# Optimization experiments

Hardware: AMD Instinct MI355X
Metric: run time of the kernel (lower is better)

The kernel has to match this reference:

```python
import jax, jax.numpy as jnp
import numpy as np

B, S, D = 2, 4096, 512
H = 8
HD = D // H


def setup_inputs() -> dict:
    key = jax.random.key(0)
    k1, k2, k3, k4, k5 = jax.random.split(key, 5)
    sd = 1.0 / np.sqrt(D)
    return {
        "x": jax.random.normal(k1, (B, S, D), dtype=jnp.float32),
        "Wqkv": jax.random.normal(k2, (3 * D, D), dtype=jnp.float32) * sd,
        "bqkv": jax.random.normal(k3, (3 * D,), dtype=jnp.float32) * 0.02,
        "Wo": jax.random.normal(k4, (D, D), dtype=jnp.float32) * sd,
        "bo": jax.random.normal(k5, (D,), dtype=jnp.float32) * 0.02,
    }


def reference(x, Wqkv, bqkv, Wo, bo):
    b, s, d = x.shape
    h, hd = H, d // H
    # QKV projection (torch Linear: x @ W^T + b)
    qkv = x @ Wqkv.T + bqkv                      # [b, s, 3d]
    q, k, v = jnp.split(qkv, 3, axis=-1)         # each [b, s, d]
    # [b, s, h, hd] -> [b, h, s, hd]
    q = q.reshape(b, s, h, hd).transpose(0, 2, 1, 3)
    k = k.reshape(b, s, h, hd).transpose(0, 2, 1, 3)
    v = v.reshape(b, s, h, hd).transpose(0, 2, 1, 3)
    # causal additive mask: triu(ones, diag=1) * -1e10
    mask = jnp.triu(jnp.ones((s, s), dtype=x.dtype), k=1) * jnp.asarray(-1e10, x.dtype)
    wts = jnp.einsum("bhqd,bhkd->bhqk", q, k) / np.sqrt(hd).astype(np.float32)
    wts = wts + mask[None, None, :, :]
    wts = jax.nn.softmax(wts, axis=-1)
    y = jnp.einsum("bhqk,bhkd->bhqd", wts, v)    # [b, h, s, hd]
    y = y.transpose(0, 2, 1, 3).reshape(b, s, d) # [b, s, d]
    out = y @ Wo.T + bo
    return out
```

## Files before the change

kernel.cpp:

```cpp
#include <hip/hip_runtime.h>


typedef __bf16 bf16x8 __attribute__((ext_vector_type(8)));
typedef float f32x4 __attribute__((ext_vector_type(4)));
typedef unsigned short u16;

#define MFMA(a, b, c) __builtin_amdgcn_mfma_f32_16x16x32_bf16(a, b, c, 0, 0, 0)
#define QSCALE 0.18033688011112042f

__device__ __forceinline__ float exp2_fast(float x) {
    return __builtin_amdgcn_exp2f(x);
}
__device__ __forceinline__ u16 f2bf(float f) {
    union { __bf16 h; u16 u; } v; v.h = (__bf16)f; return v.u;
}
__device__ __forceinline__ ushort4 f4_to_bf4(float4 v) {
    ushort4 r;
    r.x = f2bf(v.x); r.y = f2bf(v.y); r.z = f2bf(v.z); r.w = f2bf(v.w);
    return r;
}
__device__ __forceinline__ void load_lds16(const u16* g, u16* l) {
    __builtin_amdgcn_global_load_lds(
        (const __attribute__((address_space(1))) void*)g,
        (__attribute__((address_space(3))) void*)l, 16, 0, 0);
}

__global__ __launch_bounds__(256) void cvt_all(
    const float* __restrict__ x, const float* __restrict__ wq,
    const float* __restrict__ wo,
    u16* __restrict__ xb, u16* __restrict__ wqb, u16* __restrict__ wob)
{
    int i = blockIdx.x * 256 + threadIdx.x;
    if (i < 1048576) {
        ((ushort4*)xb)[i] = f4_to_bf4(((const float4*)x)[i]);
    } else if (i < 1048576 + 196608) {
        int j = i - 1048576;
        ((ushort4*)wqb)[j] = f4_to_bf4(((const float4*)wq)[j]);
    } else {
        int j = i - 1048576 - 196608;
        ((ushort4*)wob)[j] = f4_to_bf4(((const float4*)wo)[j]);
    }
}

__global__ __launch_bounds__(256) void gemm_qkv_bf(
    const u16* __restrict__ X, const u16* __restrict__ W,
    const float* __restrict__ bias,
    u16* __restrict__ QY, u16* __restrict__ Ko, u16* __restrict__ Vto)
{
    __shared__ u16 As[2 * 128 * 32];
    __shared__ u16 Bs[2 * 128 * 32];
    const int K = 512;
    const int tid = threadIdx.x, wave = tid >> 6, lane = tid & 63;
    const int l15 = lane & 15, quad = lane >> 4;
    const int bm = blockIdx.x * 128, bn = blockIdx.y * 128;
    const int wr = wave >> 1, wc = wave & 1;
    const int arow = lane >> 2;
    const int acol = (lane & 3) * 8;

    f32x4 acc[4][4] = {};
#pragma unroll
    for (int ii = 0; ii < 2; ii++) {
        const int inst = wave * 2 + ii;
        const int row = inst * 16 + arow;
        load_lds16(&X[(bm + row) * K + acol], &As[inst * 512]);
        load_lds16(&W[(bn + row) * K + acol], &Bs[inst * 512]);
    }
    int cur = 0;
    for (int k0 = 0; k0 < K; k0 += 32) {
        __builtin_amdgcn_s_barrier();
        if (k0 + 32 < K) {
            const int nb = (cur ^ 1) * 4096;
#pragma unroll
            for (int ii = 0; ii < 2; ii++) {
                const int inst = wave * 2 + ii;
                const int row = inst * 16 + arow;
                load_lds16(&X[(bm + row) * K + k0 + 32 + acol], &As[nb + inst * 512]);
                load_lds16(&W[(bn + row) * K + k0 + 32 + acol], &Bs[nb + inst * 512]);
            }
            asm volatile("s_waitcnt vmcnt(4)" ::: "memory");
        } else {
            asm volatile("s_waitcnt vmcnt(0)" ::: "memory");
        }
        __builtin_amdgcn_s_barrier();
        const int cb = cur * 4096;
        bf16x8 a[4], b[4];
#pragma unroll
        for (int i = 0; i < 4; i++)
            a[i] = *(const bf16x8*)&As[cb + (wr * 64 + i * 16 + l15) * 32 + quad * 8];
#pragma unroll
        for (int j = 0; j < 4; j++)
            b[j] = *(const bf16x8*)&Bs[cb + (wc * 64 + j * 16 + l15) * 32 + quad * 8];
#pragma unroll
        for (int i = 0; i < 4; i++)
#pragma unroll
            for (int j = 0; j < 4; j++)
                acc[i][j] = MFMA(b[i], a[j], acc[i][j]);
        cur ^= 1;
    }

    const int nbase = bn + wc * 64;
    const int which = nbase >> 9;
#pragma unroll
    for (int i = 0; i < 4; i++) {
        const int d0 = nbase + i * 16 + quad * 4;
        const float4 bv = *(const float4*)&bias[d0];
        const int d0m = d0 & 511;
        const int h = d0m >> 6, hd0 = d0m & 63;
#pragma unroll
        for (int j = 0; j < 4; j++) {
            const int s_g = bm + wr * 64 + j * 16 + l15;
            const int b_ = s_g >> 12, s0 = s_g & 4095;
            const int bhh = b_ * 8 + h;
            if (which == 2) {
#pragma unroll
                for (int r = 0; r < 4; r++) {
                    const float bvr = (r == 0) ? bv.x : (r == 1) ? bv.y : (r == 2) ? bv.z : bv.w;
                    Vto[((size_t)(bhh * 64 + hd0 + r)) * 4096 + s0] = f2bf(acc[i][j][r] + bvr);
                }
            } else if (which == 1) {
                ushort4 pk;
                pk.x = f2bf(acc[i][j][0] + bv.x);
                pk.y = f2bf(acc[i][j][1] + bv.y);
                pk.z = f2bf(acc[i][j][2] + bv.z);
                pk.w = f2bf(acc[i][j][3] + bv.w);
                *(ushort4*)&Ko[(bhh * 4096 + s0) * 64 + hd0] = pk;
            } else {
                ushort4 pk;
                pk.x = f2bf((acc[i][j][0] + bv.x) * QSCALE);
                pk.y = f2bf((acc[i][j][1] + bv.y) * QSCALE);
                pk.z = f2bf((acc[i][j][2] + bv.z) * QSCALE);
                pk.w = f2bf((acc[i][j][3] + bv.w) * QSCALE);
                *(ushort4*)&QY[((b_ * 4096 + s0) * 8 + h) * 64 + hd0] = pk;
            }
        }
    }
}

#define LS 72

__global__ __launch_bounds__(128, 4) void attn_k(
    const u16* __restrict__ QY, const u16* __restrict__ Kk, const u16* __restrict__ Vt,
    u16* __restrict__ PO, float* __restrict__ ML)
{
    __shared__ u16 Ks[2 * 64 * 64];
    __shared__ u16 Vs[64 * 64];
    __shared__ u16 Ps[2 * 16 * LS];

    const int tid = threadIdx.x, wave = tid >> 6, lane = tid & 63;
    const int l15 = lane & 15, quad = lane >> 4;
    const int bh = blockIdx.x;
    const int b_ = bh >> 3, h = bh & 7;
    const int y = (int)blockIdx.y;
    const int qt = 63 - (y >> 1);
    const int seg = y & 1;
    const int total = qt + 1;
    const int half = (total + 1) >> 1;
    const int kt0 = seg ? half : 0;
    const int kt1 = seg ? total : half;
    const int base_r = qt * 64 + wave * 32;

    const u16* qpa = &QY[((b_ * 4096 + base_r + l15) * 8 + h) * 64];
    const u16* qpb = qpa + 16 * 8 * 64;
    bf16x8 qa0 = *(const bf16x8*)&qpa[quad * 8];
    bf16x8 qa1 = *(const bf16x8*)&qpa[32 + quad * 8];
    bf16x8 qb0 = *(const bf16x8*)&qpb[quad * 8];
    bf16x8 qb1 = *(const bf16x8*)&qpb[32 + quad * 8];

    f32x4 oa[4] = {}, ob[4] = {};
    f32x4 lacc_a = {}, lacc_b = {};

    const int sr = lane >> 3;
    const int swz = 8 * ((lane & 7) ^ sr);
    const u16* KgA = &Kk[(size_t)bh * 4096 * 64 + (wave * 32 + sr) * 64 + swz];
    const u16* VgA = &Vt[(size_t)bh * 64 * 4096 + (wave * 32 + sr) * 4096 + swz];
    u16* KsW = &Ks[wave * 2048];
    u16* VsW = &Vs[wave * 2048];

    const int c0 = 8 * (quad ^ (l15 & 7));

    bf16x8 ones;
#pragma unroll
    for (int i = 0; i < 8; i++) ones[i] = (__bf16)1.0f;

    u16* P = &Ps[wave * 16 * LS];

#pragma unroll
    for (int i = 0; i < 4; i++)
        load_lds16(KgA + kt0 * 4096 + i * 512, KsW + i * 512);

    int cur = 0;
    for (int kt = kt0; kt < kt1; kt++) {
        const int k0 = kt * 64;
        __builtin_amdgcn_s_barrier();
#pragma unroll
        for (int i = 0; i < 4; i++)
            load_lds16(VgA + k0 + i * 32768, VsW + i * 512);
        const bool havnext = (kt + 1 < kt1);
        if (havnext) {
            u16* kb = &Ks[(cur ^ 1) * 4096 + wave * 2048];
#pragma unroll
            for (int i = 0; i < 4; i++)
                load_lds16(KgA + (kt + 1) * 4096 + i * 512, kb + i * 512);
            asm volatile("s_waitcnt vmcnt(8)" ::: "memory");
        } else {
            asm volatile("s_waitcnt vmcnt(4)" ::: "memory");
        }
        __builtin_amdgcn_s_barrier();

        const u16* Kcur = &Ks[cur * 4096];
        const bool nmA = (k0 + 63 > base_r);
        const bool nmB = (k0 + 63 > base_r + 16);
        f32x4 sa[4], sb[4];
#pragma unroll
        for (int j = 0; j < 4; j++) {
            f32x4 ia = {}, ib = {};
            if (nmA) {
#pragma unroll
                for (int r = 0; r < 4; r++) {
                    const int key = k0 + j * 16 + quad * 4 + r;
                    ia[r] = (key > base_r + l15) ? -1e30f : 0.0f;
                }
            }
            if (nmB) {
#pragma unroll
                for (int r = 0; r < 4; r++) {
                    const int key = k0 + j * 16 + quad * 4 + r;
                    ib[r] = (key > base_r + 16 + l15) ? -1e30f : 0.0f;
                }
            }
            const int kb = (j * 16 + l15) * 64;
            bf16x8 kf0 = *(const bf16x8*)&Kcur[kb + c0];
            bf16x8 kf1 = *(const bf16x8*)&Kcur[kb + (c0 ^ 32)];
            ia = MFMA(kf0, qa0, ia);
            sa[j] = MFMA(kf1, qa1, ia);
            ib = MFMA(kf0, qb0, ib);
            sb[j] = MFMA(kf1, qb1, ib);
        }

        {
            float spa[4][4];
#pragma unroll
            for (int j = 0; j < 4; j++)
#pragma unroll
                for (int r = 0; r < 4; r++)
                    spa[j][r] = exp2_fast(sa[j][r]);
#pragma unroll
            for (int j = 0; j < 4; j++) {
                ushort4 w;
                w.x = f2bf(spa[j][0]); w.y = f2bf(spa[j][1]);
                w.z = f2bf(spa[j][2]); w.w = f2bf(spa[j][3]);
                *(ushort4*)&P[l15 * LS + j * 16 + quad * 4] = w;
            }
        }

        float spb[4][4];
#pragma unroll
        for (int j = 0; j < 4; j++)
#pragma unroll
            for (int r = 0; r < 4; r++)
                spb[j][r] = exp2_fast(sb[j][r]);

        bf16x8 pfa0 = *(const bf16x8*)&P[l15 * LS + quad * 8];
        bf16x8 pfa1 = *(const bf16x8*)&P[l15 * LS + 32 + quad * 8];
#pragma unroll
        for (int j = 0; j < 4; j++) {
            ushort4 w;
            w.x = f2bf(spb[j][0]); w.y = f2bf(spb[j][1]);
            w.z = f2bf(spb[j][2]); w.w = f2bf(spb[j][3]);
            *(ushort4*)&P[l15 * LS + j * 16 + quad * 4] = w;
        }
        bf16x8 pfb0 = *(const bf16x8*)&P[l15 * LS + quad * 8];
        bf16x8 pfb1 = *(const bf16x8*)&P[l15 * LS + 32 + quad * 8];

        lacc_a = MFMA(ones, pfa0, lacc_a);
        lacc_a = MFMA(ones, pfa1, lacc_a);
        lacc_b = MFMA(ones, pfb0, lacc_b);
        lacc_b = MFMA(ones, pfb1, lacc_b);

        if (havnext) {
            asm volatile("s_waitcnt vmcnt(4)" ::: "memory");
        } else {
            asm volatile("s_waitcnt vmcnt(0)" ::: "memory");
        }
        __builtin_amdgcn_s_barrier();

#pragma unroll
        for (int n = 0; n < 4; n++) {
            const int vb = (n * 16 + l15) * 64;
            bf16x8 vf0 = *(const bf16x8*)&Vs[vb + c0];
            bf16x8 vf1 = *(const bf16x8*)&Vs[vb + (c0 ^ 32)];
            oa[n] = MFMA(vf0, pfa0, oa[n]);
            oa[n] = MFMA(vf1, pfa1, oa[n]);
            ob[n] = MFMA(vf0, pfb0, ob[n]);
            ob[n] = MFMA(vf1, pfb1, ob[n]);
        }
        cur ^= 1;
    }

    const float lfa = lacc_a[0];
    const float lfb = lacc_b[0];
    const float iva = (lfa > 0.0f) ? 1.0f / lfa : 0.0f;
    const float ivb = (lfb > 0.0f) ? 1.0f / lfb : 0.0f;
    u16* ppa = &PO[(size_t)seg * 4194304 +
                   (size_t)((b_ * 4096 + base_r + l15) * 8 + h) * 64];
    u16* ppb = ppa + 16 * 8 * 64;
#pragma unroll
    for (int n = 0; n < 4; n++) {
        ushort4 wa;
        wa.x = f2bf(oa[n][0] * iva);
        wa.y = f2bf(oa[n][1] * iva);
        wa.z = f2bf(oa[n][2] * iva);
        wa.w = f2bf(oa[n][3] * iva);
        *(ushort4*)&ppa[n * 16 + quad * 4] = wa;
        ushort4 wb;
        wb.x = f2bf(ob[n][0] * ivb);
        wb.y = f2bf(ob[n][1] * ivb);
        wb.z = f2bf(ob[n][2] * ivb);
        wb.w = f2bf(ob[n][3] * ivb);
        *(ushort4*)&ppb[n * 16 + quad * 4] = wb;
    }
    if (quad == 0) {
        float* mpa = &ML[((seg * 16 + bh) * 4096 + base_r + l15) * 2];
        mpa[0] = 0.0f;
        mpa[1] = lfa;
        float* mpb = mpa + 16 * 2;
        mpb[0] = 0.0f;
        mpb[1] = lfb;
    }
}

__global__ __launch_bounds__(256) void merge_k(
    const u16* __restrict__ PO, const float* __restrict__ ML, u16* __restrict__ Y)
{
    const int flat = blockIdx.x * 256 + threadIdx.x;
    const int rs = flat >> 6;
    const int rem = flat & 63;
    const int h = rem >> 3, c = rem & 7;
    const int b_ = rs >> 12, s = rs & 4095;
    const int bh = b_ * 8 + h;
    const float m0 = ML[(bh * 4096 + s) * 2];
    const float l0 = ML[(bh * 4096 + s) * 2 + 1];
    const float m1 = ML[((16 + bh) * 4096 + s) * 2];
    const float l1 = ML[((16 + bh) * 4096 + s) * 2 + 1];
    const float m = fmaxf(m0, m1);
    const float w0 = (l0 > 0.0f) ? exp2_fast(m0 - m) * l0 : 0.0f;
    const float w1 = (l1 > 0.0f) ? exp2_fast(m1 - m) * l1 : 0.0f;
    const float inv = 1.0f / (w0 + w1);
    const float a0 = w0 * inv, a1 = w1 * inv;

    const size_t base = (size_t)(rs * 8 + h) * 64 + c * 8;
    bf16x8 x0 = *(const bf16x8*)&PO[base];
    bf16x8 x1 = *(const bf16x8*)&PO[4194304 + base];
    ushort4 lo, hi;
    lo.x = f2bf(a0 * (float)x0[0] + a1 * (float)x1[0]);
    lo.y = f2bf(a0 * (float)x0[1] + a1 * (float)x1[1]);
    lo.z = f2bf(a0 * (float)x0[2] + a1 * (float)x1[2]);
    lo.w = f2bf(a0 * (float)x0[3] + a1 * (float)x1[3]);
    hi.x = f2bf(a0 * (float)x0[4] + a1 * (float)x1[4]);
    hi.y = f2bf(a0 * (float)x0[5] + a1 * (float)x1[5]);
    hi.z = f2bf(a0 * (float)x0[6] + a1 * (float)x1[6]);
    hi.w = f2bf(a0 * (float)x0[7] + a1 * (float)x1[7]);
    *(ushort4*)&Y[base] = lo;
    *(ushort4*)&Y[base + 4] = hi;
}

__global__ __launch_bounds__(256) void gemm_o_bf(
    const u16* __restrict__ X, const u16* __restrict__ W,
    const float* __restrict__ bias, float* __restrict__ Out)
{
    __shared__ u16 As[2 * 128 * 32];
    __shared__ u16 Bs[2 * 128 * 32];
    const int K = 512;
    const int tid = threadIdx.x, wave = tid >> 6, lane = tid & 63;
    const int l15 = lane & 15, quad = lane >> 4;
    const int bm = blockIdx.x * 128, bn = blockIdx.y * 128;
    const int wr = wave >> 1, wc = wave & 1;
    const int arow = lane >> 2;
    const int acol = (lane & 3) * 8;

    f32x4 acc[4][4] = {};
#pragma unroll
    for (int ii = 0; ii < 2; ii++) {
        const int inst = wave * 2 + ii;
        const int row = inst * 16 + arow;
        load_lds16(&X[(bm + row) * K + acol], &As[inst * 512]);
        load_lds16(&W[(bn + row) * K + acol], &Bs[inst * 512]);
    }
    int cur = 0;
    for (int k0 = 0; k0 < K; k0 += 32) {
        __builtin_amdgcn_s_barrier();
        if (k0 + 32 < K) {
            const int nb = (cur ^ 1) * 4096;
#pragma unroll
            for (int ii = 0; ii < 2; ii++) {
                const int inst = wave * 2 + ii;
                const int row = inst * 16 + arow;
                load_lds16(&X[(bm + row) * K + k0 + 32 + acol], &As[nb + inst * 512]);
                load_lds16(&W[(bn + row) * K + k0 + 32 + acol], &Bs[nb + inst * 512]);
            }
            asm volatile("s_waitcnt vmcnt(4)" ::: "memory");
        } else {
            asm volatile("s_waitcnt vmcnt(0)" ::: "memory");
        }
        __builtin_amdgcn_s_barrier();
        const int cb = cur * 4096;
        bf16x8 a[4], b[4];
#pragma unroll
        for (int i = 0; i < 4; i++)
            a[i] = *(const bf16x8*)&As[cb + (wr * 64 + i * 16 + l15) * 32 + quad * 8];
#pragma unroll
        for (int j = 0; j < 4; j++)
            b[j] = *(const bf16x8*)&Bs[cb + (wc * 64 + j * 16 + l15) * 32 + quad * 8];
#pragma unroll
        for (int i = 0; i < 4; i++)
#pragma unroll
            for (int j = 0; j < 4; j++)
                acc[i][j] = MFMA(b[i], a[j], acc[i][j]);
        cur ^= 1;
    }
#pragma unroll
    for (int i = 0; i < 4; i++) {
        const int n0 = bn + wc * 64 + i * 16 + quad * 4;
        const float4 bv = *(const float4*)&bias[n0];
#pragma unroll
        for (int j = 0; j < 4; j++) {
            const int m = bm + wr * 64 + j * 16 + l15;
            float4 ov;
            ov.x = acc[i][j][0] + bv.x;
            ov.y = acc[i][j][1] + bv.y;
            ov.z = acc[i][j][2] + bv.z;
            ov.w = acc[i][j][3] + bv.w;
            *(float4*)&Out[(size_t)m * 512 + n0] = ov;
        }
    }
}

extern "C" void kernel_launch(void* const* d_in, const int* in_sizes, int n_in,
                              void* d_out, int out_size, void* d_ws, size_t ws_size,
                              hipStream_t stream) {
    (void)in_sizes; (void)n_in; (void)out_size; (void)ws_size;
    const float* x    = (const float*)d_in[0];
    const float* Wqkv = (const float*)d_in[1];
    const float* bqkv = (const float*)d_in[2];
    const float* Wo   = (const float*)d_in[3];
    const float* bo   = (const float*)d_in[4];
    float* out = (float*)d_out;

    u16* qy_ws = (u16*)d_ws;
    u16* k_ws  = qy_ws + 4194304;
    u16* vt_ws = k_ws + 4194304;
    float* ml  = (float*)(vt_ws + 4194304);
    u16* wqkvb = (u16*)(ml + 262144);
    u16* wob   = wqkvb + 786432;
    u16* xb    = (u16*)d_out;
    u16* po    = (u16*)d_out;

    cvt_all<<<5120, 256, 0, stream>>>(x, Wqkv, Wo, xb, wqkvb, wob);
    gemm_qkv_bf<<<dim3(64, 12), 256, 0, stream>>>(xb, wqkvb, bqkv, qy_ws, k_ws, vt_ws);
    attn_k<<<dim3(16, 128), 128, 0, stream>>>(qy_ws, k_ws, vt_ws, po, ml);
    merge_k<<<2048, 256, 0, stream>>>(po, ml, qy_ws);
    gemm_o_bf<<<dim3(64, 4), 256, 0, stream>>>(qy_ws, wob, bo, out);
}
```

Baseline: 182.1 us.

## Store K/V in MFMA-fragment layout and load directly from global in single-wave attention

The QKV GEMM epilogue now writes K and V in a per-64-key-tile layout that matches the MFMA operand fragments, so each lane reads its fragments with contiguous 16-byte global loads. The attention kernel drops the LDS staging, double buffering and barriers, runs one wave per block, and gives each block two 32-row query tiles paired from opposite ends of the causal triangle to balance work. This removes LDS traffic and block synchronisation, but loses K/V reuse across waves and leaves global latency unhidden except by occupancy.

```diff
diff --git a/kernel.cpp b/kernel.cpp
--- a/kernel.cpp
+++ b/kernel.cpp
@@ -45,7 +45,7 @@
 __global__ __launch_bounds__(256) void gemm_qkv_bf(
     const u16* __restrict__ X, const u16* __restrict__ W,
     const float* __restrict__ bias,
-    u16* __restrict__ QY, u16* __restrict__ Ko, u16* __restrict__ Vto)
+    u16* __restrict__ QY, u16* __restrict__ Kf, u16* __restrict__ Vf)
 {
     __shared__ u16 As[2 * 128 * 32];
     __shared__ u16 Bs[2 * 128 * 32];
@@ -111,19 +111,30 @@
             const int s_g = bm + wr * 64 + j * 16 + l15;
             const int b_ = s_g >> 12, s0 = s_g & 4095;
             const int bhh = b_ * 8 + h;
+            const int kt = s0 >> 6;
             if (which == 2) {
+                const int kk = s0 & 63;
+                const int halfv = kk >> 5, qv = (kk >> 3) & 3, e = kk & 7;
+                const int n = hd0 >> 4;
+                const int lv0 = hd0 & 15;
+                const size_t tb = ((size_t)(bhh * 64 + kt)) * 4096 +
+                                  n * 1024 + halfv * 512 + qv * 128 + e;
 #pragma unroll
                 for (int r = 0; r < 4; r++) {
                     const float bvr = (r == 0) ? bv.x : (r == 1) ? bv.y : (r == 2) ? bv.z : bv.w;
-                    Vto[((size_t)(bhh * 64 + hd0 + r)) * 4096 + s0] = f2bf(acc[i][j][r] + bvr);
+                    Vf[tb + (lv0 + r) * 8] = f2bf(acc[i][j][r] + bvr);
                 }
             } else if (which == 1) {
+                const int jj = (s0 >> 4) & 3, lr = s0 & 15;
+                const int half = hd0 >> 5, q4 = (hd0 >> 3) & 3, e0 = hd0 & 7;
                 ushort4 pk;
                 pk.x = f2bf(acc[i][j][0] + bv.x);
                 pk.y = f2bf(acc[i][j][1] + bv.y);
                 pk.z = f2bf(acc[i][j][2] + bv.z);
                 pk.w = f2bf(acc[i][j][3] + bv.w);
-                *(ushort4*)&Ko[(bhh * 4096 + s0) * 64 + hd0] = pk;
+                const size_t off = ((size_t)(bhh * 64 + kt)) * 4096 +
+                                   jj * 1024 + half * 512 + q4 * 128 + lr * 8 + e0;
+                *(ushort4*)&Kf[off] = pk;
             } else {
                 ushort4 pk;
                 pk.x = f2bf((acc[i][j][0] + bv.x) * QSCALE);
@@ -138,194 +149,170 @@
 
 #define LS 72
 
-__global__ __launch_bounds__(128, 4) void attn_k(
-    const u16* __restrict__ QY, const u16* __restrict__ Kk, const u16* __restrict__ Vt,
+__global__ __launch_bounds__(64, 3) void attn_k(
+    const u16* __restrict__ QY, const u16* __restrict__ Kf, const u16* __restrict__ Vf,
     u16* __restrict__ PO, float* __restrict__ ML)
 {
-    __shared__ u16 Ks[2 * 64 * 64];
-    __shared__ u16 Vs[64 * 64];
-    __shared__ u16 Ps[2 * 16 * LS];
-
-    const int tid = threadIdx.x, wave = tid >> 6, lane = tid & 63;
+    __shared__ u16 Ps[16 * LS];
+
+    const int lane = threadIdx.x;
     const int l15 = lane & 15, quad = lane >> 4;
     const int bh = blockIdx.x;
     const int b_ = bh >> 3, h = bh & 7;
     const int y = (int)blockIdx.y;
-    const int qt = 63 - (y >> 1);
+    const int p = y >> 1;
     const int seg = y & 1;
-    const int total = qt + 1;
-    const int half = (total + 1) >> 1;
-    const int kt0 = seg ? half : 0;
-    const int kt1 = seg ? total : half;
-    const int base_r = qt * 64 + wave * 32;
-
-    const u16* qpa = &QY[((b_ * 4096 + base_r + l15) * 8 + h) * 64];
-    const u16* qpb = qpa + 16 * 8 * 64;
-    bf16x8 qa0 = *(const bf16x8*)&qpa[quad * 8];
-    bf16x8 qa1 = *(const bf16x8*)&qpa[32 + quad * 8];
-    bf16x8 qb0 = *(const bf16x8*)&qpb[quad * 8];
-    bf16x8 qb1 = *(const bf16x8*)&qpb[32 + quad * 8];
-
-    f32x4 oa[4] = {}, ob[4] = {};
-    f32x4 lacc_a = {}, lacc_b = {};
-
-    const int sr = lane >> 3;
-    const int swz = 8 * ((lane & 7) ^ sr);
-    const u16* KgA = &Kk[(size_t)bh * 4096 * 64 + (wave * 32 + sr) * 64 + swz];
-    const u16* VgA = &Vt[(size_t)bh * 64 * 4096 + (wave * 32 + sr) * 4096 + swz];
-    u16* KsW = &Ks[wave * 2048];
-    u16* VsW = &Vs[wave * 2048];
-
-    const int c0 = 8 * (quad ^ (l15 & 7));
 
     bf16x8 ones;
 #pragma unroll
     for (int i = 0; i < 8; i++) ones[i] = (__bf16)1.0f;
 
-    u16* P = &Ps[wave * 16 * LS];
-
-#pragma unroll
-    for (int i = 0; i < 4; i++)
-        load_lds16(KgA + kt0 * 4096 + i * 512, KsW + i * 512);
-
-    int cur = 0;
-    for (int kt = kt0; kt < kt1; kt++) {
-        const int k0 = kt * 64;
-        __builtin_amdgcn_s_barrier();
-#pragma unroll
-        for (int i = 0; i < 4; i++)
-            load_lds16(VgA + k0 + i * 32768, VsW + i * 512);
-        const bool havnext = (kt + 1 < kt1);
-        if (havnext) {
-            u16* kb = &Ks[(cur ^ 1) * 4096 + wave * 2048];
-#pragma unroll
-            for (int i = 0; i < 4; i++)
-                load_lds16(KgA + (kt + 1) * 4096 + i * 512, kb + i * 512);
-            asm volatile("s_waitcnt vmcnt(8)" ::: "memory");
-        } else {
-            asm volatile("s_waitcnt vmcnt(4)" ::: "memory");
-        }
-        __builtin_amdgcn_s_barrier();
-
-        const u16* Kcur = &Ks[cur * 4096];
-        const bool nmA = (k0 + 63 > base_r);
-        const bool nmB = (k0 + 63 > base_r + 16);
-        f32x4 sa[4], sb[4];
-#pragma unroll
-        for (int j = 0; j < 4; j++) {
-            f32x4 ia = {}, ib = {};
-            if (nmA) {
-#pragma unroll
-                for (int r = 0; r < 4; r++) {
-                    const int key = k0 + j * 16 + quad * 4 + r;
-                    ia[r] = (key > base_r + l15) ? -1e30f : 0.0f;
+    const u16* KfB = &Kf[((size_t)bh * 64) * 4096 + lane * 8];
+    const u16* VfB = &Vf[((size_t)bh * 64) * 4096 + lane * 8];
+    u16* P = Ps;
+
+    for (int phase = 0; phase < 2; phase++) {
+        const int qt32 = phase ? (127 - p) : p;
+        const int nt = (qt32 >> 1) + 1;
+        const int hlf = (nt + 1) >> 1;
+        const int t0 = seg ? hlf : 0;
+        const int t1 = seg ? nt : hlf;
+        const int base_r = qt32 * 32;
+
+        const u16* qpa = &QY[((b_ * 4096 + base_r + l15) * 8 + h) * 64];
+        const u16* qpb = qpa + 16 * 8 * 64;
+        bf16x8 qa0 = *(const bf16x8*)&qpa[quad * 8];
+        bf16x8 qa1 = *(const bf16x8*)&qpa[32 + quad * 8];
+        bf16x8 qb0 = *(const bf16x8*)&qpb[quad * 8];
+        bf16x8 qb1 = *(const bf16x8*)&qpb[32 + quad * 8];
+
+        f32x4 oa[4] = {}, ob[4] = {};
+        f32x4 lacc_a = {}, lacc_b = {};
+        const int rowA = base_r + l15;
+
+        for (int kt = t0; kt < t1; kt++) {
+            const int k0 = kt * 64;
+            const u16* kp = KfB + kt * 4096;
+
+            bf16x8 kf[4][2];
+#pragma unroll
+            for (int j = 0; j < 4; j++) {
+                kf[j][0] = *(const bf16x8*)&kp[j * 1024];
+                kf[j][1] = *(const bf16x8*)&kp[j * 1024 + 512];
+            }
+
+            const bool nmA = (k0 + 63 > base_r);
+            const bool nmB = (k0 + 63 > base_r + 16);
+            f32x4 sa[4], sb[4];
+#pragma unroll
+            for (int j = 0; j < 4; j++) {
+                f32x4 ia = {}, ib = {};
+                if (nmA) {
+#pragma unroll
+                    for (int r = 0; r < 4; r++) {
+                        const int key = k0 + j * 16 + quad * 4 + r;
+                        ia[r] = (key > rowA) ? -1e30f : 0.0f;
+                    }
                 }
-            }
-            if (nmB) {
-#pragma unroll
-                for (int r = 0; r < 4; r++) {
-                    const int key = k0 + j * 16 + quad * 4 + r;
-                    ib[r] = (key > base_r + 16 + l15) ? -1e30f : 0.0f;
+                if (nmB) {
+#pragma unroll
+                    for (int r = 0; r < 4; r++) {
+                        const int key = k0 + j * 16 + quad * 4 + r;
+                        ib[r] = (key > rowA + 16) ? -1e30f : 0.0f;
+                    }
                 }
-            }
-            const int kb = (j * 16 + l15) * 64;
-            bf16x8 kf0 = *(const bf16x8*)&Kcur[kb + c0];
-            bf16x8 kf1 = *(const bf16x8*)&Kcur[kb + (c0 ^ 32)];
-            ia = MFMA(kf0, qa0, ia);
-            sa[j] = MFMA(kf1, qa1, ia);
-            ib = MFMA(kf0, qb0, ib);
-            sb[j] = MFMA(kf1, qb1, ib);
-        }
-
-        {
-            float spa[4][4];
+                ia = MFMA(kf[j][0], qa0, ia);
+                sa[j] = MFMA(kf[j][1], qa1, ia);
+                ib = MFMA(kf[j][0], qb0, ib);
+                sb[j] = MFMA(kf[j][1], qb1, ib);
+            }
+
+            const u16* vp = VfB + kt * 4096;
+            bf16x8 vf[4][2];
+#pragma unroll
+            for (int n = 0; n < 4; n++) {
+                vf[n][0] = *(const bf16x8*)&vp[n * 1024];
+                vf[n][1] = *(const bf16x8*)&vp[n * 1024 + 512];
+            }
+
+            {
+                float spa[4][4];
+#pragma unroll
+                for (int j = 0; j < 4; j++)
+#pragma unroll
+                    for (int r = 0; r < 4; r++)
+                        spa[j][r] = exp2_fast(sa[j][r]);
+#pragma unroll
+                for (int j = 0; j < 4; j++) {
+                    ushort4 w;
+                    w.x = f2bf(spa[j][0]); w.y = f2bf(spa[j][1]);
+                    w.z = f2bf(spa[j][2]); w.w = f2bf(spa[j][3]);
+                    *(ushort4*)&P[l15 * LS + j * 16 + quad * 4] = w;
+                }
+            }
+            float spb[4][4];
 #pragma unroll
             for (int j = 0; j < 4; j++)
 #pragma unroll
                 for (int r = 0; r < 4; r++)
-                    spa[j][r] = exp2_fast(sa[j][r]);
+                    spb[j][r] = exp2_fast(sb[j][r]);
+
+            bf16x8 pfa0 = *(const bf16x8*)&P[l15 * LS + quad * 8];
+            bf16x8 pfa1 = *(const bf16x8*)&P[l15 * LS + 32 + quad * 8];
 #pragma unroll
             for (int j = 0; j < 4; j++) {
                 ushort4 w;
-                w.x = f2bf(spa[j][0]); w.y = f2bf(spa[j][1]);
-                w.z = f2bf(spa[j][2]); w.w = f2bf(spa[j][3]);
+                w.x = f2bf(spb[j][0]); w.y = f2bf(spb[j][1]);
+                w.z = f2bf(spb[j][2]); w.w = f2bf(spb[j][3]);
                 *(ushort4*)&P[l15 * LS + j * 16 + quad * 4] = w;
             }
-        }
-
-        float spb[4][4];
-#pragma unroll
-        for (int j = 0; j < 4; j++)
-#pragma unroll
-            for (int r = 0; r < 4; r++)
-                spb[j][r] = exp2_fast(sb[j][r]);
-
-        bf16x8 pfa0 = *(const bf16x8*)&P[l15 * LS + quad * 8];
-        bf16x8 pfa1 = *(const bf16x8*)&P[l15 * LS + 32 + quad * 8];
-#pragma unroll
-        for (int j = 0; j < 4; j++) {
-            ushort4 w;
-            w.x = f2bf(spb[j][0]); w.y = f2bf(spb[j][1]);
-            w.z = f2bf(spb[j][2]); w.w = f2bf(spb[j][3]);
-            *(ushort4*)&P[l15 * LS + j * 16 + quad * 4] = w;
-        }
-        bf16x8 pfb0 = *(const bf16x8*)&P[l15 * LS + quad * 8];
-        bf16x8 pfb1 = *(const bf16x8*)&P[l15 * LS + 32 + quad * 8];
-
-        lacc_a = MFMA(ones, pfa0, lacc_a);
-        lacc_a = MFMA(ones, pfa1, lacc_a);
-        lacc_b = MFMA(ones, pfb0, lacc_b);
-        lacc_b = MFMA(ones, pfb1, lacc_b);
-
-        if (havnext) {
-            asm volatile("s_waitcnt vmcnt(4)" ::: "memory");
-        } else {
-            asm volatile("s_waitcnt vmcnt(0)" ::: "memory");
-        }
-        __builtin_amdgcn_s_barrier();
-
+            bf16x8 pfb0 = *(const bf16x8*)&P[l15 * LS + quad * 8];
+            bf16x8 pfb1 = *(const bf16x8*)&P[l15 * LS + 32 + quad * 8];
+
+            lacc_a = MFMA(ones, pfa0, lacc_a);
+            lacc_a = MFMA(ones, pfa1, lacc_a);
+            lacc_b = MFMA(ones, pfb0, lacc_b);
+            lacc_b = MFMA(ones, pfb1, lacc_b);
+
+#pragma unroll
+            for (int n = 0; n < 4; n++) {
+                oa[n] = MFMA(vf[n][0], pfa0, oa[n]);
+                oa[n] = MFMA(vf[n][1], pfa1, oa[n]);
+                ob[n] = MFMA(vf[n][0], pfb0, ob[n]);
+                ob[n] = MFMA(vf[n][1], pfb1, ob[n]);
+            }
+        }
+
+        const float lfa = lacc_a[0];
+        const float lfb = lacc_b[0];
+        const float iva = (lfa > 0.0f) ? 1.0f / lfa : 0.0f;
+        const float ivb = (lfb > 0.0f) ? 1.0f / lfb : 0.0f;
+        u16* ppa = &PO[(size_t)seg * 4194304 +
+                       (size_t)((b_ * 4096 + base_r + l15) * 8 + h) * 64];
+        u16* ppb = ppa + 16 * 8 * 64;
 #pragma unroll
         for (int n = 0; n < 4; n++) {
-            const int vb = (n * 16 + l15) * 64;
-            bf16x8 vf0 = *(const bf16x8*)&Vs[vb + c0];
-            bf16x8 vf1 = *(const bf16x8*)&Vs[vb + (c0 ^ 32)];
-            oa[n] = MFMA(vf0, pfa0, oa[n]);
-            oa[n] = MFMA(vf1, pfa1, oa[n]);
-            ob[n] = MFMA(vf0, pfb0, ob[n]);
-            ob[n] = MFMA(vf1, pfb1, ob[n]);
-        }
-        cur ^= 1;
-    }
-
-    const float lfa = lacc_a[0];
-    const float lfb = lacc_b[0];
-    const float iva = (lfa > 0.0f) ? 1.0f / lfa : 0.0f;
-    const float ivb = (lfb > 0.0f) ? 1.0f / lfb : 0.0f;
-    u16* ppa = &PO[(size_t)seg * 4194304 +
-                   (size_t)((b_ * 4096 + base_r + l15) * 8 + h) * 64];
-    u16* ppb = ppa + 16 * 8 * 64;
-#pragma unroll
-    for (int n = 0; n < 4; n++) {
-        ushort4 wa;
-        wa.x = f2bf(oa[n][0] * iva);
-        wa.y = f2bf(oa[n][1] * iva);
-        wa.z = f2bf(oa[n][2] * iva);
-        wa.w = f2bf(oa[n][3] * iva);
-        *(ushort4*)&ppa[n * 16 + quad * 4] = wa;
-        ushort4 wb;
-        wb.x = f2bf(ob[n][0] * ivb);
-        wb.y = f2bf(ob[n][1] * ivb);
-        wb.z = f2bf(ob[n][2] * ivb);
-        wb.w = f2bf(ob[n][3] * ivb);
-        *(ushort4*)&ppb[n * 16 + quad * 4] = wb;
-    }
-    if (quad == 0) {
-        float* mpa = &ML[((seg * 16 + bh) * 4096 + base_r + l15) * 2];
-        mpa[0] = 0.0f;
-        mpa[1] = lfa;
-        float* mpb = mpa + 16 * 2;
-        mpb[0] = 0.0f;
-        mpb[1] = lfb;
+            ushort4 wa;
+            wa.x = f2bf(oa[n][0] * iva);
+            wa.y = f2bf(oa[n][1] * iva);
+            wa.z = f2bf(oa[n][2] * iva);
+            wa.w = f2bf(oa[n][3] * iva);
+            *(ushort4*)&ppa[n * 16 + quad * 4] = wa;
+            ushort4 wb;
+            wb.x = f2bf(ob[n][0] * ivb);
+            wb.y = f2bf(ob[n][1] * ivb);
+            wb.z = f2bf(ob[n][2] * ivb);
+            wb.w = f2bf(ob[n][3] * ivb);
+            *(ushort4*)&ppb[n * 16 + quad * 4] = wb;
+        }
+        if (quad == 0) {
+            float* mpa = &ML[((seg * 16 + bh) * 4096 + base_r + l15) * 2];
+            mpa[0] = 0.0f;
+            mpa[1] = lfa;
+            float* mpb = mpa + 16 * 2;
+            mpb[0] = 0.0f;
+            mpb[1] = lfb;
+        }
     }
 }
 
@@ -447,17 +434,17 @@
     float* out = (float*)d_out;
 
     u16* qy_ws = (u16*)d_ws;
-    u16* k_ws  = qy_ws + 4194304;
-    u16* vt_ws = k_ws + 4194304;
-    float* ml  = (float*)(vt_ws + 4194304);
+    u16* kf_ws = qy_ws + 4194304;
+    u16* vf_ws = kf_ws + 4194304;
+    float* ml  = (float*)(vf_ws + 4194304);
     u16* wqkvb = (u16*)(ml + 262144);
     u16* wob   = wqkvb + 786432;
     u16* xb    = (u16*)d_out;
     u16* po    = (u16*)d_out;
 
     cvt_all<<<5120, 256, 0, stream>>>(x, Wqkv, Wo, xb, wqkvb, wob);
-    gemm_qkv_bf<<<dim3(64, 12), 256, 0, stream>>>(xb, wqkvb, bqkv, qy_ws, k_ws, vt_ws);
-    attn_k<<<dim3(16, 128), 128, 0, stream>>>(qy_ws, k_ws, vt_ws, po, ml);
+    gemm_qkv_bf<<<dim3(64, 12), 256, 0, stream>>>(xb, wqkvb, bqkv, qy_ws, kf_ws, vf_ws);
+    attn_k<<<dim3(16, 128), 64, 0, stream>>>(qy_ws, kf_ws, vf_ws, po, ml);
     merge_k<<<2048, 256, 0, stream>>>(po, ml, qy_ws);
     gemm_o_bf<<<dim3(64, 4), 256, 0, stream>>>(qy_ws, wob, bo, out);
 }
```

New measurement: 179.4 us. About the same (-1.5%).
